# Kernel optimization log

Hardware: AMD Instinct MI355X
Metric: run time of the kernel (lower is better)

Reference implementation:

```python
import jax, jax.numpy as jnp
import numpy as np

B, T, C, H, DFF = 4, 1024, 1024, 16, 4096
HS = C // H  # 64
EPS = 1e-5


def layer_norm(x, g, b):
    mu = jnp.mean(x, axis=-1, keepdims=True)
    var = jnp.var(x, axis=-1, keepdims=True)
    return (x - mu) * jax.lax.rsqrt(var + EPS) * g + b


def setup_inputs() -> dict:
    key = jax.random.key(0)
    ks = jax.random.split(key, 12)
    s = 0.02
    return {
        "x": jax.random.normal(ks[0], (B, T, C), jnp.float32),
        "wq": jax.random.normal(ks[1], (H, C, HS), jnp.float32) * s,
        "wk": jax.random.normal(ks[2], (H, C, HS), jnp.float32) * s,
        "wv": jax.random.normal(ks[3], (H, C, HS), jnp.float32) * s,
        "w_proj": jax.random.normal(ks[4], (H * HS, C), jnp.float32) * s,
        "b_proj": jnp.zeros((C,), jnp.float32),
        "w1": jax.random.normal(ks[5], (C, DFF), jnp.float32) * s,
        "b1": jnp.zeros((DFF,), jnp.float32),
        "w2": jax.random.normal(ks[6], (DFF, C), jnp.float32) * s,
        "b2": jnp.zeros((C,), jnp.float32),
        "g1": jnp.ones((C,), jnp.float32),
        "be1": jnp.zeros((C,), jnp.float32),
        "g2": jnp.ones((C,), jnp.float32),
        "be2": jnp.zeros((C,), jnp.float32),
    }


def reference(x, wq, wk, wv, w_proj, b_proj, w1, b1, w2, b2, g1, be1, g2, be2):
    h = layer_norm(x, g1, be1)
    # per-head projections, vectorized over heads: [B,H,T,HS]
    q = jnp.einsum('btc,hcd->bhtd', h, wq)
    k = jnp.einsum('btc,hcd->bhtd', h, wk)
    v = jnp.einsum('btc,hcd->bhtd', h, wv)
    # mask=None in the original forward, so no causal masking
    wei = jnp.einsum('bhtd,bhsd->bhts', q, k) * (HS ** -0.5)
    wei = jax.nn.softmax(wei, axis=-1)  # [B,H,T,T]
    out = jnp.einsum('bhts,bhsd->bhtd', wei, v)
    out = out.transpose(0, 2, 1, 3).reshape(B, T, H * HS)  # concat heads
    attn_out = out @ w_proj + b_proj
    x = x + attn_out
    h2 = layer_norm(x, g2, be2)
    ff = jax.nn.relu(h2 @ w1 + b1) @ w2 + b2
    x = x + ff
    return x, wei
```

## Files before the change

kernel.cpp:

```cpp
#include <hip/hip_runtime.h>
#include <hip/hip_bf16.h>

#define BB    4
#define TT    1024
#define CC    1024
#define HH    16
#define HSZ   64
#define DFF   4096
#define NTOK  (BB*TT)
#define BHN   (BB*HH)

typedef __attribute__((ext_vector_type(8))) short bf16x8;
typedef __attribute__((ext_vector_type(4))) float f32x4;

#define VMC0 asm volatile("s_waitcnt vmcnt(0)" ::: "memory")
#define VMC4 asm volatile("s_waitcnt vmcnt(4)" ::: "memory")
#define LGK0 asm volatile("s_waitcnt lgkmcnt(0)" ::: "memory")
#define BARRIER do { asm volatile("" ::: "memory"); \
                     __builtin_amdgcn_s_barrier();  \
                     asm volatile("" ::: "memory"); } while (0)

__device__ __forceinline__ ushort f2b(float v) {
    union { float f; unsigned u; } c; c.f = v;
    unsigned r = c.u + 0x7fffu + ((c.u >> 16) & 1u);
    return (ushort)(r >> 16);
}
__device__ __forceinline__ void stv(float* p, float v)  { *p = v; }
__device__ __forceinline__ void stv(ushort* p, float v) { *p = f2b(v); }

__device__ __forceinline__ void gload16(const void* g, void* l) {
    __builtin_amdgcn_global_load_lds(
        (const __attribute__((address_space(1))) void*)g,
        (__attribute__((address_space(3))) void*)l, 16, 0, 0);
}

__global__ __launch_bounds__(256)
void ln_k(const float* __restrict__ x, const float* __restrict__ g,
          const float* __restrict__ be, ushort* __restrict__ o)
{
    __shared__ float s1[4], s2[4];
    long row = blockIdx.x;
    const float4* xr = (const float4*)(x + row * CC);
    float4 v = xr[threadIdx.x];
    float a = v.x + v.y + v.z + v.w;
    float b = v.x*v.x + v.y*v.y + v.z*v.z + v.w*v.w;
    for (int off = 32; off > 0; off >>= 1) {
        a += __shfl_down(a, off);
        b += __shfl_down(b, off);
    }
    if ((threadIdx.x & 63) == 0) { s1[threadIdx.x >> 6] = a; s2[threadIdx.x >> 6] = b; }
    __syncthreads();
    float sum = s1[0] + s1[1] + s1[2] + s1[3];
    float sq  = s2[0] + s2[1] + s2[2] + s2[3];
    float mu  = sum * (1.0f / CC);
    float var = sq * (1.0f / CC) - mu * mu;
    float inv = rsqrtf(var + 1e-5f);
    float4 gg = ((const float4*)g)[threadIdx.x];
    float4 bb = ((const float4*)be)[threadIdx.x];
    ushort4 r;
    r.x = f2b((v.x - mu) * inv * gg.x + bb.x);
    r.y = f2b((v.y - mu) * inv * gg.y + bb.y);
    r.z = f2b((v.z - mu) * inv * gg.z + bb.z);
    r.w = f2b((v.w - mu) * inv * gg.w + bb.w);
    ((ushort4*)(o + row * CC))[threadIdx.x] = r;
}

__global__ __launch_bounds__(256)
void cvtall_k(const float* __restrict__ wq, const float* __restrict__ wk,
              const float* __restrict__ wv, const float* __restrict__ wproj,
              const float* __restrict__ w1, const float* __restrict__ w2,
              ushort* __restrict__ wqkvT, ushort* __restrict__ wpT,
              ushort* __restrict__ w1T, ushort* __restrict__ w2T)
{
    __shared__ float t[32][33];
    int idx = blockIdx.x;
    const float* src; ushort* dst; int R, Cc, bx, by;
    if (idx < 3072) {
        int seg = idx >> 10, rem = idx & 1023;
        int z = rem >> 6, tt2 = rem & 63;
        src = (seg == 0 ? wq : seg == 1 ? wk : wv) + (long)z * 65536;
        dst = wqkvT + (long)seg * (1L << 20) + (long)z * 65536;
        R = 1024; Cc = 64; bx = tt2 & 1; by = tt2 >> 1;
    } else if (idx < 4096) {
        int tt2 = idx - 3072;
        src = wproj; dst = wpT; R = 1024; Cc = 1024; bx = tt2 & 31; by = tt2 >> 5;
    } else if (idx < 8192) {
        int tt2 = idx - 4096;
        src = w1; dst = w1T; R = 1024; Cc = 4096; bx = tt2 & 127; by = tt2 >> 7;
    } else {
        int tt2 = idx - 8192;
        src = w2; dst = w2T; R = 4096; Cc = 1024; bx = tt2 & 31; by = tt2 >> 5;
    }
    int r0 = by * 32, c0 = bx * 32;
    int tx = threadIdx.x & 31, ty = threadIdx.x >> 5;
#pragma unroll
    for (int i = 0; i < 4; i++)
        t[ty + 8*i][tx] = src[(long)(r0 + ty + 8*i) * Cc + c0 + tx];
    __syncthreads();
#pragma unroll
    for (int i = 0; i < 4; i++)
        dst[(long)(c0 + ty + 8*i) * R + r0 + tx] = f2b(t[tx][ty + 8*i]);
}

enum { OL_PLAIN = 0, OL_QKV3 = 1 };
constexpr int EBIAS = 1, ERELU = 2, ERES = 4, ESCALE = 8;

template<int BM, int BN, int WM, int WN, int OL, int EPI, typename OutT>
__global__ __launch_bounds__(256)
void mgemm_k(const ushort* __restrict__ A, const ushort* __restrict__ Bt,
             const float* __restrict__ bias, const float* __restrict__ res,
             OutT* __restrict__ C, int M, int N, int K,
             long sA, long sB, long sC, float scale)
{
    constexpr int BK = 64;
    constexpr int FM = BM / WM / 16, FN = BN / WN / 16;
    __shared__ ushort As[BM * BK];
    __shared__ ushort Bs[BN * BK];
    const int tid = threadIdx.x;
    const int w = tid >> 6, l = tid & 63;
    const int wr = w / WN, wc = w % WN;
    const int l15 = l & 15, l4 = l >> 4;
    const int bh = blockIdx.z;
    const ushort* Ap = A  + (long)bh * sA + (long)(blockIdx.y * BM) * K;
    const ushort* Bp = Bt + (long)bh * sB + (long)(blockIdx.x * BN) * K;

    f32x4 acc[FM][FN];
#pragma unroll
    for (int m = 0; m < FM; m++)
#pragma unroll
        for (int n = 0; n < FN; n++) acc[m][n] = (f32x4){0.f, 0.f, 0.f, 0.f};

    const int arow = tid >> 3;
    const int achk = tid & 7;

    for (int k0 = 0; k0 < K; k0 += BK) {
#pragma unroll
        for (int i = 0; i < BM / 32; i++)
            gload16(Ap + (long)(i*32 + arow) * K + k0 + achk*8,
                    &As[(i*32 + w*8) * BK]);
#pragma unroll
        for (int i = 0; i < BN / 32; i++)
            gload16(Bp + (long)(i*32 + arow) * K + k0 + achk*8,
                    &Bs[(i*32 + w*8) * BK]);
        __syncthreads();
#pragma unroll
        for (int kk = 0; kk < 2; kk++) {
            const int ko = kk*32 + l4*8;
            bf16x8 af[FM], bfr[FN];
#pragma unroll
            for (int m = 0; m < FM; m++)
                af[m] = *(const bf16x8*)&As[(wr*(BM/WM) + m*16 + l15) * BK + ko];
#pragma unroll
            for (int n = 0; n < FN; n++)
                bfr[n] = *(const bf16x8*)&Bs[(wc*(BN/WN) + n*16 + l15) * BK + ko];
#pragma unroll
            for (int m = 0; m < FM; m++)
#pragma unroll
                for (int n = 0; n < FN; n++)
                    acc[m][n] = __builtin_amdgcn_mfma_f32_16x16x32_bf16(
                        af[m], bfr[n], acc[m][n], 0, 0, 0);
        }
        __syncthreads();
    }

#pragma unroll
    for (int m = 0; m < FM; m++) {
        int rbase = blockIdx.y*BM + wr*(BM/WM) + m*16 + l4*4;
#pragma unroll
        for (int n = 0; n < FN; n++) {
            int col = blockIdx.x*BN + wc*(BN/WN) + n*16 + l15;
#pragma unroll
            for (int r = 0; r < 4; r++) {
                int row = rbase + r;
                float v = acc[m][n][r];
                if (EPI & ESCALE) v *= scale;
                if (EPI & EBIAS)  v += bias[col];
                if (EPI & ERELU)  v = fmaxf(v, 0.f);
                if (EPI & ERES)   v += res[(long)row * N + col];
                long idx;
                if (OL == OL_PLAIN) {
                    idx = (long)row * N + col;
                } else {
                    int seg = col >> 10;
                    int cl  = col & 1023;
                    long bh_ = ((long)((row >> 10) * HH + (cl >> 6))) * 65536;
                    long off = (seg == 2)
                        ? bh_ + (long)(cl & 63) * 1024 + (row & 1023)
                        : bh_ + (long)(row & 1023) * 64 + (cl & 63);
                    idx = (long)seg * (4L << 20) + off;
                }
                stv(&C[(long)bh * sC + idx], v);
            }
        }
    }
}

__global__ __launch_bounds__(256, 2)
void fattn_k(const ushort* __restrict__ q_, const ushort* __restrict__ k_,
             const ushort* __restrict__ vt, float* __restrict__ wei,
             ushort* __restrict__ attn)
{
    __shared__ ushort Qs[128*64];
    __shared__ ushort Ks[128*64];
    __shared__ ushort Vs[64*128];
    __shared__ ushort Ps[128*128];
    float* sred = (float*)Ps;

    const int tid = threadIdx.x;
    const int w = tid >> 6, l = tid & 63;
    const int wr = w >> 1, wc = w & 1;
    const int l15 = l & 15, l4 = l >> 4;
    const int bh = blockIdx.y;
    const int q0 = blockIdx.x * 128;
    const int arow = tid >> 3, achk = tid & 7;
    const int kchk = achk ^ (arow & 7);
    const int vrow = tid >> 4;
    const int vchk = (tid & 15) ^ (vrow & 15);
    const int sw8  = (l15 & 7) << 3;
    const int sw16 = l15 << 3;

    const ushort* Qp = q_ + (long)bh * 65536;
    const ushort* Kp = k_ + (long)bh * 65536;
    const ushort* Vp = vt + (long)bh * 65536;

#pragma unroll
    for (int i = 0; i < 4; i++)
        gload16(Qp + (long)(q0 + i*32 + arow) * 64 + kchk*8, &Qs[(i*32 + w*8)*64]);
#pragma unroll
    for (int i = 0; i < 4; i++)
        gload16(Kp + (long)(i*32 + arow) * 64 + kchk*8, &Ks[(i*32 + w*8)*64]);

    float ssum[4][4];
#pragma unroll
    for (int m = 0; m < 4; m++)
#pragma unroll
        for (int r = 0; r < 4; r++) ssum[m][r] = 0.f;

    for (int st = 0; st < 8; ++st) {
        const ushort* cur = (st & 1) ? Vs : Ks;
        ushort*       nxt = (st & 1) ? Ks : Vs;
        if (st < 7) {
#pragma unroll
            for (int i = 0; i < 4; i++)
                gload16(Kp + (long)((st+1)*128 + i*32 + arow) * 64 + kchk*8,
                        &nxt[(i*32 + w*8)*64]);
            VMC4;
        } else {
            VMC0;
        }
        BARRIER;

        f32x4 sacc[4][4];
#pragma unroll
        for (int m = 0; m < 4; m++)
#pragma unroll
            for (int n = 0; n < 4; n++) sacc[m][n] = (f32x4){0.f,0.f,0.f,0.f};
        __builtin_amdgcn_s_setprio(1);
#pragma unroll
        for (int kk = 0; kk < 2; kk++) {
            const int ko = kk*32 + l4*8;
            bf16x8 af[4], bfr[4];
#pragma unroll
            for (int m = 0; m < 4; m++)
                af[m] = *(const bf16x8*)&Qs[(wr*64 + m*16 + l15)*64 + (ko ^ sw8)];
#pragma unroll
            for (int n = 0; n < 4; n++)
                bfr[n] = *(const bf16x8*)&cur[(wc*64 + n*16 + l15)*64 + (ko ^ sw8)];
#pragma unroll
            for (int m = 0; m < 4; m++)
#pragma unroll
                for (int n = 0; n < 4; n++)
                    sacc[m][n] = __builtin_amdgcn_mfma_f32_16x16x32_bf16(
                        af[m], bfr[n], sacc[m][n], 0, 0, 0);
        }
        __builtin_amdgcn_s_setprio(0);
#pragma unroll
        for (int m = 0; m < 4; m++)
#pragma unroll
            for (int r = 0; r < 4; r++) {
                float s = 0.f;
#pragma unroll
                for (int n = 0; n < 4; n++) s += __expf(sacc[m][n][r] * 0.125f);
                ssum[m][r] += s;
            }
        BARRIER;
    }

#pragma unroll
    for (int i = 0; i < 4; i++)
        gload16(Kp + (long)(i*32 + arow) * 64 + kchk*8, &Ks[(i*32 + w*8)*64]);
#pragma unroll
    for (int i = 0; i < 4; i++)
        gload16(Vp + (long)(i*16 + vrow) * 1024 + vchk*8, &Vs[(i*16 + w*4)*128]);

    float linv[4][4];
#pragma unroll
    for (int m = 0; m < 4; m++)
#pragma unroll
        for (int r = 0; r < 4; r++) {
            float s = ssum[m][r];
#pragma unroll
            for (int d = 1; d < 16; d <<= 1) s += __shfl_xor(s, d);
            if (l15 == 0) sred[wc*128 + wr*64 + m*16 + l4*4 + r] = s;
        }
    LGK0; BARRIER;
#pragma unroll
    for (int m = 0; m < 4; m++)
#pragma unroll
        for (int r = 0; r < 4; r++) {
            int rg = wr*64 + m*16 + l4*4 + r;
            linv[m][r] = 1.0f / (sred[rg] + sred[128 + rg]);
        }

    f32x4 oacc[4][2];
#pragma unroll
    for (int m = 0; m < 4; m++)
#pragma unroll
        for (int n = 0; n < 2; n++) oacc[m][n] = (f32x4){0.f,0.f,0.f,0.f};

    for (int st = 0; st < 8; ++st) {
        if (st > 0) {
#pragma unroll
            for (int i = 0; i < 4; i++)
                gload16(Kp + (long)(st*128 + i*32 + arow) * 64 + kchk*8,
                        &Ks[(i*32 + w*8)*64]);
#pragma unroll
            for (int i = 0; i < 4; i++)
                gload16(Vp + (long)(i*16 + vrow) * 1024 + st*128 + vchk*8,
                        &Vs[(i*16 + w*4)*128]);
        }
        VMC0;
        BARRIER;

        f32x4 sacc[4][4];
#pragma unroll
        for (int m = 0; m < 4; m++)
#pragma unroll
            for (int n = 0; n < 4; n++) sacc[m][n] = (f32x4){0.f,0.f,0.f,0.f};
        __builtin_amdgcn_s_setprio(1);
#pragma unroll
        for (int kk = 0; kk < 2; kk++) {
            const int ko = kk*32 + l4*8;
            bf16x8 af[4], bfr[4];
#pragma unroll
            for (int m = 0; m < 4; m++)
                af[m] = *(const bf16x8*)&Qs[(wr*64 + m*16 + l15)*64 + (ko ^ sw8)];
#pragma unroll
            for (int n = 0; n < 4; n++)
                bfr[n] = *(const bf16x8*)&Ks[(wc*64 + n*16 + l15)*64 + (ko ^ sw8)];
#pragma unroll
            for (int m = 0; m < 4; m++)
#pragma unroll
                for (int n = 0; n < 4; n++)
                    sacc[m][n] = __builtin_amdgcn_mfma_f32_16x16x32_bf16(
                        af[m], bfr[n], sacc[m][n], 0, 0, 0);
        }
        __builtin_amdgcn_s_setprio(0);

        float pv[4][4][4];
#pragma unroll
        for (int m = 0; m < 4; m++)
#pragma unroll
            for (int r = 0; r < 4; r++) {
                int rg = wr*64 + m*16 + l4*4 + r;
                int psw = (rg & 15) << 3;
                float li = linv[m][r];
#pragma unroll
                for (int n = 0; n < 4; n++) {
                    int col = wc*64 + n*16 + l15;
                    float p = __expf(sacc[m][n][r] * 0.125f) * li;
                    pv[m][n][r] = p;
                    Ps[rg*128 + (col ^ psw)] = f2b(p);
                }
            }
        LGK0; BARRIER;

        __builtin_amdgcn_s_setprio(1);
#pragma unroll
        for (int kc = 0; kc < 4; ++kc) {
            const int ko = kc*32 + l4*8;
            bf16x8 pa[4], vb[2];
#pragma unroll
            for (int m = 0; m < 4; m++)
                pa[m] = *(const bf16x8*)&Ps[(wr*64 + m*16 + l15)*128 + (ko ^ sw16)];
#pragma unroll
            for (int n = 0; n < 2; n++)
                vb[n] = *(const bf16x8*)&Vs[(wc*32 + n*16 + l15)*128 + (ko ^ sw16)];
#pragma unroll
            for (int m = 0; m < 4; m++)
#pragma unroll
                for (int n = 0; n < 2; n++)
                    oacc[m][n] = __builtin_amdgcn_mfma_f32_16x16x32_bf16(
                        pa[m], vb[n], oacc[m][n], 0, 0, 0);
        }
        __builtin_amdgcn_s_setprio(0);

        float* wrow = wei + (long)bh * (TT*(long)TT) + st*128;
#pragma unroll
        for (int m = 0; m < 4; m++)
#pragma unroll
            for (int r = 0; r < 4; r++) {
                int rg = wr*64 + m*16 + l4*4 + r;
#pragma unroll
                for (int n = 0; n < 4; n++) {
                    int col = wc*64 + n*16 + l15;
                    __builtin_nontemporal_store(pv[m][n][r],
                        &wrow[(long)(q0 + rg) * TT + col]);
                }
            }
        BARRIER;
    }

#pragma unroll
    for (int m = 0; m < 4; m++)
#pragma unroll
        for (int r = 0; r < 4; r++) {
            int rg = wr*64 + m*16 + l4*4 + r;
            long rowbase = ((long)(bh >> 4) * TT + q0 + rg) * CC + (long)(bh & 15) * HSZ;
#pragma unroll
            for (int n = 0; n < 2; n++)
                attn[rowbase + wc*32 + n*16 + l15] = f2b(oacc[m][n][r]);
        }
}

extern "C" void kernel_launch(void* const* d_in, const int* in_sizes, int n_in,
                              void* d_out, int out_size, void* d_ws, size_t ws_size,
                              hipStream_t stream)
{
    const float* x      = (const float*)d_in[0];
    const float* wq     = (const float*)d_in[1];
    const float* wk     = (const float*)d_in[2];
    const float* wv     = (const float*)d_in[3];
    const float* w_proj = (const float*)d_in[4];
    const float* b_proj = (const float*)d_in[5];
    const float* w1     = (const float*)d_in[6];
    const float* b1     = (const float*)d_in[7];
    const float* w2     = (const float*)d_in[8];
    const float* b2     = (const float*)d_in[9];
    const float* g1     = (const float*)d_in[10];
    const float* be1    = (const float*)d_in[11];
    const float* g2     = (const float*)d_in[12];
    const float* be2    = (const float*)d_in[13];

    float* out_x = (float*)d_out;
    float* wei   = out_x + (long)NTOK * CC;

    const long MEL = 1 << 20;
    ushort* ws16 = (ushort*)d_ws;
    ushort* h    = ws16;
    ushort* q_   = ws16 + 4*MEL;
    ushort* k_   = ws16 + 8*MEL;
    ushort* vt   = ws16 + 12*MEL;
    ushort* attn = ws16 + 16*MEL;
    ushort* h2   = ws16 + 20*MEL;
    ushort* a1   = ws16 + 24*MEL;
    ushort* wqkvT= ws16 + 40*MEL;
    ushort* w1T  = ws16 + 44*MEL;
    ushort* wpT  = ws16 + 48*MEL;
    ushort* w2T  = ws16 + 49*MEL;
    float*  x1   = (float*)(ws16 + 54*MEL);

    cvtall_k<<<12288, 256, 0, stream>>>(wq, wk, wv, w_proj, w1, w2,
                                        wqkvT, wpT, w1T, w2T);

    ln_k<<<NTOK, 256, 0, stream>>>(x, g1, be1, h);

    mgemm_k<128,128,2,2,OL_QKV3,0,ushort><<<dim3(24,32,1), 256, 0, stream>>>(
        h, wqkvT, nullptr, nullptr, q_, NTOK, 3072, CC, 0,0,0, 0.f);

    fattn_k<<<dim3(8, 64), 256, 0, stream>>>(q_, k_, vt, wei, attn);

    mgemm_k<128,128,2,2,OL_PLAIN,EBIAS|ERES,float><<<dim3(8,32,1), 256, 0, stream>>>(
        attn, wpT, b_proj, x, x1, NTOK, CC, CC, 0,0,0, 0.f);

    ln_k<<<NTOK, 256, 0, stream>>>(x1, g2, be2, h2);

    mgemm_k<128,128,2,2,OL_PLAIN,EBIAS|ERELU,ushort><<<dim3(32,32,1), 256, 0, stream>>>(
        h2, w1T, b1, nullptr, a1, NTOK, DFF, CC, 0,0,0, 0.f);

    mgemm_k<128,128,2,2,OL_PLAIN,EBIAS|ERES,float><<<dim3(8,32,1), 256, 0, stream>>>(
        a1, w2T, b2, x1, out_x, NTOK, CC, DFF, 0,0,0, 0.f);
}
```

Baseline: 369.4 us.

## Double-buffer GEMM LDS tiles and defer attention weight stores past next loads

The GEMM kernel now uses two LDS buffers and prefetches the next K tile with global_load_lds before computing the current one. It waits with a partial vmcnt so the new loads stay in flight while the MFMAs run. In the attention kernel, the store of the previous stage's softmax probabilities is moved to just after the next K/V loads are issued, and a vmcnt(48) wait lets those stores drain in the background; the nontemporal hint is dropped. This is meant to hide global load latency and the large wei write traffic behind compute, at the cost of double the GEMM LDS footprint and pv registers kept live across iterations. The vmcnt thresholds are hand-tuned and must match the exact number of outstanding memory ops, which is fragile.

```diff
diff --git a/kernel.cpp b/kernel.cpp
--- a/kernel.cpp
+++ b/kernel.cpp
@@ -13,9 +13,11 @@
 typedef __attribute__((ext_vector_type(8))) short bf16x8;
 typedef __attribute__((ext_vector_type(4))) float f32x4;
 
-#define VMC0 asm volatile("s_waitcnt vmcnt(0)" ::: "memory")
-#define VMC4 asm volatile("s_waitcnt vmcnt(4)" ::: "memory")
-#define LGK0 asm volatile("s_waitcnt lgkmcnt(0)" ::: "memory")
+#define VMC0  asm volatile("s_waitcnt vmcnt(0)" ::: "memory")
+#define VMC4  asm volatile("s_waitcnt vmcnt(4)" ::: "memory")
+#define VMC8  asm volatile("s_waitcnt vmcnt(8)" ::: "memory")
+#define VMC48 asm volatile("s_waitcnt vmcnt(48)" ::: "memory")
+#define LGK0  asm volatile("s_waitcnt lgkmcnt(0)" ::: "memory")
 #define BARRIER do { asm volatile("" ::: "memory"); \
                      __builtin_amdgcn_s_barrier();  \
                      asm volatile("" ::: "memory"); } while (0)
@@ -114,8 +116,8 @@
 {
     constexpr int BK = 64;
     constexpr int FM = BM / WM / 16, FN = BN / WN / 16;
-    __shared__ ushort As[BM * BK];
-    __shared__ ushort Bs[BN * BK];
+    __shared__ ushort As[2][BM * BK];
+    __shared__ ushort Bs[2][BN * BK];
     const int tid = threadIdx.x;
     const int w = tid >> 6, l = tid & 63;
     const int wr = w / WN, wc = w % WN;
@@ -133,26 +135,41 @@
     const int arow = tid >> 3;
     const int achk = tid & 7;
 
-    for (int k0 = 0; k0 < K; k0 += BK) {
+    auto stage = [&](int buf, int kt) {
+        const int k0 = kt * BK;
 #pragma unroll
         for (int i = 0; i < BM / 32; i++)
             gload16(Ap + (long)(i*32 + arow) * K + k0 + achk*8,
-                    &As[(i*32 + w*8) * BK]);
+                    &As[buf][(i*32 + w*8) * BK]);
 #pragma unroll
         for (int i = 0; i < BN / 32; i++)
             gload16(Bp + (long)(i*32 + arow) * K + k0 + achk*8,
-                    &Bs[(i*32 + w*8) * BK]);
-        __syncthreads();
+                    &Bs[buf][(i*32 + w*8) * BK]);
+    };
+
+    const int NK = K / BK;
+    stage(0, 0);
+    for (int kt = 0; kt < NK; ++kt) {
+        const int cur = kt & 1;
+        if (kt + 1 < NK) {
+            stage(cur ^ 1, kt + 1);
+            VMC8;
+        } else {
+            VMC0;
+        }
+        BARRIER;
+        const ushort* Ac = As[cur];
+        const ushort* Bc = Bs[cur];
 #pragma unroll
         for (int kk = 0; kk < 2; kk++) {
             const int ko = kk*32 + l4*8;
             bf16x8 af[FM], bfr[FN];
 #pragma unroll
             for (int m = 0; m < FM; m++)
-                af[m] = *(const bf16x8*)&As[(wr*(BM/WM) + m*16 + l15) * BK + ko];
+                af[m] = *(const bf16x8*)&Ac[(wr*(BM/WM) + m*16 + l15) * BK + ko];
 #pragma unroll
             for (int n = 0; n < FN; n++)
-                bfr[n] = *(const bf16x8*)&Bs[(wc*(BN/WN) + n*16 + l15) * BK + ko];
+                bfr[n] = *(const bf16x8*)&Bc[(wc*(BN/WN) + n*16 + l15) * BK + ko];
 #pragma unroll
             for (int m = 0; m < FM; m++)
 #pragma unroll
@@ -160,7 +177,7 @@
                     acc[m][n] = __builtin_amdgcn_mfma_f32_16x16x32_bf16(
                         af[m], bfr[n], acc[m][n], 0, 0, 0);
         }
-        __syncthreads();
+        BARRIER;
     }
 
 #pragma unroll
@@ -318,6 +335,8 @@
 #pragma unroll
         for (int n = 0; n < 2; n++) oacc[m][n] = (f32x4){0.f,0.f,0.f,0.f};
 
+    float pv[4][4][4];
+
     for (int st = 0; st < 8; ++st) {
         if (st > 0) {
 #pragma unroll
@@ -328,8 +347,22 @@
             for (int i = 0; i < 4; i++)
                 gload16(Vp + (long)(i*16 + vrow) * 1024 + st*128 + vchk*8,
                         &Vs[(i*16 + w*4)*128]);
-        }
-        VMC0;
+            float* wrow = wei + (long)bh * (TT*(long)TT) + (st-1)*128;
+#pragma unroll
+            for (int m = 0; m < 4; m++)
+#pragma unroll
+                for (int r = 0; r < 4; r++) {
+                    int rg = wr*64 + m*16 + l4*4 + r;
+#pragma unroll
+                    for (int n = 0; n < 4; n++) {
+                        int col = wc*64 + n*16 + l15;
+                        wrow[(long)(q0 + rg) * TT + col] = pv[m][n][r];
+                    }
+                }
+            VMC48;
+        } else {
+            VMC0;
+        }
         BARRIER;
 
         f32x4 sacc[4][4];
@@ -357,7 +390,6 @@
         }
         __builtin_amdgcn_s_setprio(0);
 
-        float pv[4][4][4];
 #pragma unroll
         for (int m = 0; m < 4; m++)
 #pragma unroll
@@ -394,8 +426,11 @@
                         pa[m], vb[n], oacc[m][n], 0, 0, 0);
         }
         __builtin_amdgcn_s_setprio(0);
-
-        float* wrow = wei + (long)bh * (TT*(long)TT) + st*128;
+        BARRIER;
+    }
+
+    {
+        float* wrow = wei + (long)bh * (TT*(long)TT) + 7*128;
 #pragma unroll
         for (int m = 0; m < 4; m++)
 #pragma unroll
@@ -404,11 +439,9 @@
 #pragma unroll
                 for (int n = 0; n < 4; n++) {
                     int col = wc*64 + n*16 + l15;
-                    __builtin_nontemporal_store(pv[m][n][r],
-                        &wrow[(long)(q0 + rg) * TT + col]);
+                    wrow[(long)(q0 + rg) * TT + col] = pv[m][n][r];
                 }
             }
-        BARRIER;
     }
 
 #pragma unroll
```

Measured after the change: 397.0 us. 1.07x slower.
